# Optimization experiments

Measured on AMD Instinct MI355X. Metric: run time of the kernel, lower is better.

## Reference

```python
import jax, jax.numpy as jnp
import numpy as np

B, K, IN_DIM = 32, 8, 512
N_IDX, N_LAT = 3, 7
D_IDX, D_LAT = 2 ** N_IDX, 2 ** N_LAT  # 8, 128
D = D_IDX * D_LAT  # 1024
TED = 128


def _hamiltonian_eig():
    # H_shift = (S+ + S-) kron I_latent, S+|k> = |(k+1) mod d_idx>
    S_plus = np.roll(np.eye(D_IDX, dtype=np.float64), 1, axis=0)
    H_idx = S_plus + S_plus.T
    H = np.kron(H_idx, np.eye(D_LAT, dtype=np.float64))
    w, V = np.linalg.eigh(H)  # constant, data-independent
    return jnp.asarray(w, jnp.float32), jnp.asarray(V, jnp.float32)


_EIGVALS, _EIGVECS = _hamiltonian_eig()


def setup_inputs() -> dict:
    key = jax.random.key(0)
    ks = jax.random.split(key, 8)
    return {
        "z": jax.random.normal(ks[0], (B, K, IN_DIM), jnp.float32),
        "t": jax.random.uniform(ks[1], (B,), jnp.float32),
        "W_proj": jax.random.normal(ks[2], (D_LAT, IN_DIM), jnp.float32) * (1.0 / np.sqrt(IN_DIM)),
        "b_proj": jax.random.normal(ks[3], (D_LAT,), jnp.float32) * 0.02,
        "W1": jax.random.normal(ks[4], (TED, 1), jnp.float32),
        "b1": jax.random.normal(ks[5], (TED,), jnp.float32) * 0.02,
        "W2": jax.random.normal(ks[6], (1, TED), jnp.float32) * (1.0 / np.sqrt(TED)),
        "b2": jax.random.normal(ks[7], (1,), jnp.float32) * 0.02,
    }


def reference(z, t, W_proj, b_proj, W1, b1, W2, b2):
    # Phase A.1: amplitude encoding per shot: (B,K,IN) -> (B,K,D_LAT), L2-normalized
    psi = jnp.einsum("bki,oi->bko", z, W_proj) + b_proj
    norm = jnp.clip(jnp.linalg.norm(psi, axis=-1, keepdims=True), 1e-8)
    psi = psi / norm

    # Phase A.2: multi-shot superposition, K == d_idx fills the full state
    state = psi.reshape(B, D) * (1.0 / np.sqrt(K))  # (B, D)

    # Pure-state density matrix rho = |Psi><Psi|
    rho = state[:, :, None] * state[:, None, :]  # (B, D, D)

    # lambda(t) via MLP: Linear -> SiLU -> Linear -> Tanh, scaled by 0.1
    tf = t[:, None].astype(jnp.float32)  # (B,1)
    h = tf @ W1.T + b1
    h = h * jax.nn.sigmoid(h)  # SiLU
    lam = jnp.tanh(h @ W2.T + b2)[:, 0] * 0.1  # (B,)

    # U_b = V diag(exp(-lam_b * w)) V^T  (batched, replaces per-sample loop)
    exp_diag = jnp.exp(-lam[:, None] * _EIGVALS)  # (B, D)
    U = jnp.einsum("ij,bj,kj->bik", _EIGVECS, exp_diag, _EIGVECS)  # (B,D,D)

    # rho -> U rho U^T, trace-normalize
    rho_out = jnp.einsum("bij,bjk,blk->bil", U, rho, U)
    tr = jnp.trace(rho_out, axis1=-2, axis2=-1)[:, None, None]
    rho_out = rho_out / jnp.clip(tr, 1e-8)

    # Density-matrix projection: Hermitian + eps*I + trace normalization
    rho_out = (rho_out + jnp.swapaxes(rho_out, -1, -2)) * 0.5
    rho_out = rho_out + 1e-7 * jnp.eye(D, dtype=rho_out.dtype)
    tr = jnp.trace(rho_out, axis1=-2, axis2=-1)[:, None, None]
    return rho_out / jnp.clip(tr, 1e-8)
```

## Files before the change

kernel.cpp:

```cpp
#include <hip/hip_runtime.h>

#define NB 32
#define NK 8
#define IN_DIM 512
#define DLAT 128
#define DTOT 1024

__global__ __launch_bounds__(512) void qsfm_proj(
    const float* __restrict__ z, const float* __restrict__ W_proj,
    const float* __restrict__ b_proj, float* __restrict__ psi_out)
{
    __shared__ float psi_s[DLAT];
    __shared__ float wsum[2];

    const int shot = blockIdx.x;
    const int tid  = threadIdx.x;
    const int l = tid & 63, w = tid >> 6;
    const int h = l >> 5,  m = l & 31;

    const float4* __restrict__ zb = (const float4*)(z + (size_t)shot * IN_DIM);
    const float4 za0 = zb[m], za1 = zb[m + 32], za2 = zb[m + 64], za3 = zb[m + 96];

    const int o0 = w * 16;
    float keep = 0.f;
    #pragma unroll 4
    for (int p = 0; p < 8; ++p) {
        const int r = o0 + p * 2 + h;
        const float4* __restrict__ wr = (const float4*)(W_proj + (size_t)r * IN_DIM);
        const float4 w0 = wr[m], w1 = wr[m + 32], w2 = wr[m + 64], w3 = wr[m + 96];
        float s = (w0.x * za0.x + w0.y * za0.y + w0.z * za0.z + w0.w * za0.w)
                + (w1.x * za1.x + w1.y * za1.y + w1.z * za1.z + w1.w * za1.w)
                + (w2.x * za2.x + w2.y * za2.y + w2.z * za2.z + w2.w * za2.w)
                + (w3.x * za3.x + w3.y * za3.y + w3.z * za3.z + w3.w * za3.w);
        s += __shfl_xor(s, 1);  s += __shfl_xor(s, 2);  s += __shfl_xor(s, 4);
        s += __shfl_xor(s, 8);  s += __shfl_xor(s, 16);
        if (m == p) keep = s;
    }
    if (m < 8) psi_s[o0 + 2 * m + h] = keep;
    __syncthreads();

    float psi = 0.f;
    if (tid < 128) {
        psi = psi_s[tid] + b_proj[tid];
        float s = psi * psi;
        #pragma unroll
        for (int d = 32; d; d >>= 1) s += __shfl_xor(s, d);
        if ((tid & 63) == 0) wsum[tid >> 6] = s;
    }
    __syncthreads();
    if (tid < 128) {
        const float n2 = wsum[0] + wsum[1];
        psi_out[shot * DLAT + tid] =
            psi / fmaxf(sqrtf(n2), 1e-8f) * 0.35355339059327373f;
    }
}

__global__ __launch_bounds__(256) void qsfm_mix(
    const float* __restrict__ t,
    const float* __restrict__ W1, const float* __restrict__ b1,
    const float* __restrict__ W2, const float* __restrict__ b2,
    const float* __restrict__ psi_norm,
    float* __restrict__ a_out, float* __restrict__ diag_out)
{
    __shared__ float ps[NK * 132];
    __shared__ float lamp[2];
    __shared__ float f_s[8];
    __shared__ float npart[4];

    const int b = blockIdx.x;
    const int tid = threadIdx.x;
    const int lane = tid & 63, w = tid >> 6;
    const int k = tid >> 5;
    const int e = (tid & 31) * 4;

    {
        const float4 pv = ((const float4*)(psi_norm + (size_t)b * DTOT))[tid];
        *(float4*)(ps + k * 132 + e) = pv;
    }
    if (tid < 128) {
        const float h = t[b] * W1[tid] + b1[tid];
        float ml = W2[tid] * (h / (1.f + expf(-h)));
        #pragma unroll
        for (int m = 32; m; m >>= 1) ml += __shfl_xor(ml, m);
        if (lane == 0) lamp[w] = ml;
    }
    __syncthreads();
    if (tid < 8) {
        const float lam = tanhf(lamp[0] + lamp[1] + b2[0]) * 0.1f;
        const float c4[8] = {1.f, 0.70710678118654752f, 0.f, -0.70710678118654752f,
                             -1.f, -0.70710678118654752f, 0.f, 0.70710678118654752f};
        float a8 = 0.f;
        #pragma unroll
        for (int m = 0; m < 8; ++m)
            a8 += expf(-2.f * lam * c4[m]) * c4[(m * tid) & 7];
        f_s[tid] = 0.125f * a8;
    }
    __syncthreads();

    float4 y4 = {0.f, 0.f, 0.f, 0.f};
    #pragma unroll
    for (int kp = 0; kp < NK; ++kp) {
        const float fc = f_s[(k - kp) & 7];
        const float4 p4 = *(const float4*)(ps + kp * 132 + e);
        y4.x += fc * p4.x; y4.y += fc * p4.y;
        y4.z += fc * p4.z; y4.w += fc * p4.w;
    }
    {
        float s = (y4.x * y4.x + y4.y * y4.y) + (y4.z * y4.z + y4.w * y4.w);
        #pragma unroll
        for (int m = 32; m; m >>= 1) s += __shfl_xor(s, m);
        if (lane == 0) npart[w] = s;
    }
    __syncthreads();

    const float n2  = (npart[0] + npart[1]) + (npart[2] + npart[3]);
    const float n2c = fmaxf(n2, 1e-8f);
    const float tr2 = n2 / n2c + (float)DTOT * 1e-7f;
    const float sc  = 1.f / sqrtf(n2c * tr2);
    float4 av;
    av.x = y4.x * sc; av.y = y4.y * sc; av.z = y4.z * sc; av.w = y4.w * sc;
    ((float4*)(a_out + (size_t)b * DTOT))[tid] = av;
    if (tid == 0) diag_out[b] = 1e-7f / tr2;
}

__global__ __launch_bounds__(256) void qsfm_outer(
    const float* __restrict__ a, const float* __restrict__ diag,
    float4* __restrict__ out)
{
    const int total4 = NB * DTOT * (DTOT / 4);
    const int stride = gridDim.x * blockDim.x;
    for (int idx4 = blockIdx.x * blockDim.x + threadIdx.x; idx4 < total4;
         idx4 += stride) {
        const int j4 = idx4 & (DTOT / 4 - 1);
        const int i  = (idx4 >> 8) & (DTOT - 1);
        const int b  = idx4 >> 18;
        const float ai = a[b * DTOT + i];
        const float4 aj = *(const float4*)(a + b * DTOT + j4 * 4);
        float4 v;
        v.x = ai * aj.x; v.y = ai * aj.y; v.z = ai * aj.z; v.w = ai * aj.w;
        const int dj = i - j4 * 4;
        if (dj >= 0 && dj < 4) {
            const float dd = diag[b];
            if      (dj == 0) v.x += dd;
            else if (dj == 1) v.y += dd;
            else if (dj == 2) v.z += dd;
            else              v.w += dd;
        }
        out[idx4] = v;
    }
}

extern "C" void kernel_launch(void* const* d_in, const int* in_sizes, int n_in,
                              void* d_out, int out_size, void* d_ws, size_t ws_size,
                              hipStream_t stream) {
    (void)in_sizes; (void)n_in; (void)out_size; (void)ws_size;
    const float* z  = (const float*)d_in[0];
    const float* t  = (const float*)d_in[1];
    const float* Wp = (const float*)d_in[2];
    const float* bp = (const float*)d_in[3];
    const float* W1 = (const float*)d_in[4];
    const float* b1 = (const float*)d_in[5];
    const float* W2 = (const float*)d_in[6];
    const float* b2 = (const float*)d_in[7];

    float* ws       = (float*)d_ws;
    float* psi_norm = ws;
    float* a        = psi_norm + NB * DTOT;
    float* diag     = a + NB * DTOT;

    qsfm_proj<<<NB * NK, 512, 0, stream>>>(z, Wp, bp, psi_norm);
    qsfm_mix<<<NB, 256, 0, stream>>>(t, W1, b1, W2, b2, psi_norm, a, diag);
    qsfm_outer<<<2048, 256, 0, stream>>>(a, diag, (float4*)d_out);
}
```

Baseline: 36.45 us.

## Fuse mixing stage into outer-product kernel, recomputing per row-slab block

Merges the per-batch mixing kernel into the outer-product writer. Each of 2048 blocks recomputes lambda, the circulant mix and the normalization for its batch, then writes a 16-row slab of the output from shared memory. This drops one kernel launch and the global round trip for the intermediate vector and diagonal, at the cost of 64x redundant mix computation per batch and extra shared memory per block.

```diff
diff --git a/kernel.cpp b/kernel.cpp
--- a/kernel.cpp
+++ b/kernel.cpp
@@ -55,19 +55,23 @@
     }
 }
 
-__global__ __launch_bounds__(256) void qsfm_mix(
+__global__ __launch_bounds__(256) void qsfm_mixouter(
     const float* __restrict__ t,
     const float* __restrict__ W1, const float* __restrict__ b1,
     const float* __restrict__ W2, const float* __restrict__ b2,
     const float* __restrict__ psi_norm,
-    float* __restrict__ a_out, float* __restrict__ diag_out)
+    float4* __restrict__ out)
 {
     __shared__ float ps[NK * 132];
+    __shared__ float a_s[DTOT];
     __shared__ float lamp[2];
     __shared__ float f_s[8];
     __shared__ float npart[4];
+    __shared__ float diag_sh;
 
-    const int b = blockIdx.x;
+    const int g = blockIdx.x;
+    const int b = g >> 6;
+    const int s = g & 63;
     const int tid = threadIdx.x;
     const int lane = tid & 63, w = tid >> 6;
     const int k = tid >> 5;
@@ -106,10 +110,10 @@
         y4.z += fc * p4.z; y4.w += fc * p4.w;
     }
     {
-        float s = (y4.x * y4.x + y4.y * y4.y) + (y4.z * y4.z + y4.w * y4.w);
+        float q = (y4.x * y4.x + y4.y * y4.y) + (y4.z * y4.z + y4.w * y4.w);
         #pragma unroll
-        for (int m = 32; m; m >>= 1) s += __shfl_xor(s, m);
-        if (lane == 0) npart[w] = s;
+        for (int m = 32; m; m >>= 1) q += __shfl_xor(q, m);
+        if (lane == 0) npart[w] = q;
     }
     __syncthreads();
 
@@ -119,34 +123,28 @@
     const float sc  = 1.f / sqrtf(n2c * tr2);
     float4 av;
     av.x = y4.x * sc; av.y = y4.y * sc; av.z = y4.z * sc; av.w = y4.w * sc;
-    ((float4*)(a_out + (size_t)b * DTOT))[tid] = av;
-    if (tid == 0) diag_out[b] = 1e-7f / tr2;
-}
+    ((float4*)a_s)[tid] = av;
+    if (tid == 0) diag_sh = 1e-7f / tr2;
+    __syncthreads();
 
-__global__ __launch_bounds__(256) void qsfm_outer(
-    const float* __restrict__ a, const float* __restrict__ diag,
-    float4* __restrict__ out)
-{
-    const int total4 = NB * DTOT * (DTOT / 4);
-    const int stride = gridDim.x * blockDim.x;
-    for (int idx4 = blockIdx.x * blockDim.x + threadIdx.x; idx4 < total4;
-         idx4 += stride) {
-        const int j4 = idx4 & (DTOT / 4 - 1);
-        const int i  = (idx4 >> 8) & (DTOT - 1);
-        const int b  = idx4 >> 18;
-        const float ai = a[b * DTOT + i];
-        const float4 aj = *(const float4*)(a + b * DTOT + j4 * 4);
+    const float dd = diag_sh;
+    const float4 aj = ((const float4*)a_s)[tid];
+    float4* __restrict__ outb =
+        out + ((size_t)b << 18) + (size_t)(s * 16) * 256;
+    #pragma unroll 4
+    for (int it = 0; it < 16; ++it) {
+        const int i = s * 16 + it;
+        const float ai = a_s[i];
         float4 v;
         v.x = ai * aj.x; v.y = ai * aj.y; v.z = ai * aj.z; v.w = ai * aj.w;
-        const int dj = i - j4 * 4;
+        const int dj = i - tid * 4;
         if (dj >= 0 && dj < 4) {
-            const float dd = diag[b];
             if      (dj == 0) v.x += dd;
             else if (dj == 1) v.y += dd;
             else if (dj == 2) v.z += dd;
             else              v.w += dd;
         }
-        out[idx4] = v;
+        outb[(size_t)it * 256 + tid] = v;
     }
 }
 
@@ -163,12 +161,9 @@
     const float* W2 = (const float*)d_in[6];
     const float* b2 = (const float*)d_in[7];
 
-    float* ws       = (float*)d_ws;
-    float* psi_norm = ws;
-    float* a        = psi_norm + NB * DTOT;
-    float* diag     = a + NB * DTOT;
+    float* psi_norm = (float*)d_ws;
 
     qsfm_proj<<<NB * NK, 512, 0, stream>>>(z, Wp, bp, psi_norm);
-    qsfm_mix<<<NB, 256, 0, stream>>>(t, W1, b1, W2, b2, psi_norm, a, diag);
-    qsfm_outer<<<2048, 256, 0, stream>>>(a, diag, (float4*)d_out);
+    qsfm_mixouter<<<2048, 256, 0, stream>>>(t, W1, b1, W2, b2, psi_norm,
+                                            (float4*)d_out);
 }
```

New measurement: 33.76 us. 7.4% less time.
